# Kernel tuning notes

Hardware: AMD Instinct MI355X
Metric: run time of the kernel (lower is better)

Reference implementation:

```python
import jax, jax.numpy as jnp
import numpy as np

B, L, D, H = 4, 8192, 1024, 8
Dh = D // H
EPS = 1e-4
PAD = 1  # circular padding on each side, kernel_size=3, stride=1


def setup_inputs() -> dict:
    key = jax.random.key(0)
    k1, k2, k3, k4, k5 = jax.random.split(key, 5)
    return {
        "x": jax.random.normal(k1, (B, L, D), dtype=jnp.float32),
        "hash_w": jax.random.normal(k2, (H, Dh, 2), dtype=jnp.float32) * 0.05,
        "hash_b": jax.random.normal(k3, (H, 2), dtype=jnp.float32) * 0.05,
        "conv_w": jax.random.normal(k4, (D, D // H, 3), dtype=jnp.float32) * 0.05,
        "conv_b": jax.random.normal(k5, (D,), dtype=jnp.float32) * 0.05,
    }


def reference(x, hash_w, hash_b, conv_w, conv_b):
    # x: [B, L, D]
    xh = x.reshape(B, L, H, Dh)
    # per-head 2-dim hash projection, concatenated as [x0,y0,x1,y1,...] on last dim
    proj = jnp.einsum('blhd,hdk->blhk', xh, hash_w) + hash_b  # [B,L,H,2]
    proj = proj.reshape(B, L, 2 * H)
    # faithful to torch.split(projected, n_heads, dim=2): first H vs last H channels
    h_x, h_y = proj[..., :H], proj[..., H:]
    angles = jnp.arctan(h_x / (h_y + EPS))  # [B,L,H]
    idx = jnp.argsort(angles, axis=1)       # [B,L,H] permutation along L per (b,h)
    # gather: reorder tokens per head
    xs = jnp.take_along_axis(xh, idx[..., None], axis=1)  # [B,L,H,Dh]
    # grouped circular Conv1d over the sorted sequence
    xc = xs.reshape(B, L, D).swapaxes(1, 2)               # [B,D,L]
    xc = jnp.pad(xc, ((0, 0), (0, 0), (PAD, PAD)), mode='wrap')
    y = jax.lax.conv_general_dilated(
        xc, conv_w, window_strides=(1,), padding='VALID',
        dimension_numbers=('NCH', 'OIH', 'NCH'), feature_group_count=H)
    y = y + conv_b[None, :, None]                          # [B,D,L]
    y = y.swapaxes(1, 2).reshape(B, L, H, Dh)
    # scatter back to original token order == gather with inverse permutation
    inv = jnp.argsort(idx, axis=1)
    out = jnp.take_along_axis(y, inv[..., None], axis=1)
    return out.reshape(B, L, D)
```

## Files before the change

### kernel.cpp

```cpp
#include <hip/hip_runtime.h>
#include <math.h>

#define LL 8192
#define DD 1024
#define DH 128

typedef unsigned long long u64;
typedef __attribute__((ext_vector_type(8))) short bf16x8;
typedef __attribute__((ext_vector_type(4))) float f32x4;

__device__ __forceinline__ unsigned short f2bf(float f) {
  unsigned u = __float_as_uint(f);
  u = (u + 0x7fffu + ((u >> 16) & 1u)) >> 16;
  return (unsigned short)u;
}

__device__ __forceinline__ float fdlibm_atanf(float x) {
#pragma clang fp contract(off)
  const float atanhi0 = __uint_as_float(0x3eed6338u);
  const float atanhi1 = __uint_as_float(0x3f490fdau);
  const float atanhi2 = __uint_as_float(0x3f7b985eu);
  const float atanhi3 = __uint_as_float(0x3fc90fdau);
  const float atanlo0 = __uint_as_float(0x31ac3769u);
  const float atanlo1 = __uint_as_float(0x33222168u);
  const float atanlo2 = __uint_as_float(0x33140fb4u);
  const float atanlo3 = __uint_as_float(0x33a22168u);
  const float aT0 = __uint_as_float(0x3eaaaaa9u);
  const float aT1 = __uint_as_float(0xbe4cca98u);
  const float aT2 = __uint_as_float(0x3e11f50du);
  const float aT3 = __uint_as_float(0xbdda1247u);
  const float aT4 = __uint_as_float(0x3d7cac25u);
  unsigned hx = __float_as_uint(x);
  unsigned ix = hx & 0x7fffffffu;
  int id;
  if (ix >= 0x4c800000u) {
    if (ix > 0x7f800000u) return x + x;
    float z = atanhi3 + atanlo3;
    return (hx >> 31) ? -z : z;
  }
  if (ix < 0x3ee00000u) {
    if (ix < 0x39800000u) return x;
    id = -1;
  } else {
    x = fabsf(x);
    if (ix < 0x3f980000u) {
      if (ix < 0x3f300000u) { id = 0; x = (2.0f * x - 1.0f) / (2.0f + x); }
      else                  { id = 1; x = (x - 1.0f) / (x + 1.0f); }
    } else {
      if (ix < 0x401c0000u) { id = 2; x = (x - 1.5f) / (1.0f + 1.5f * x); }
      else                  { id = 3; x = -1.0f / x; }
    }
  }
  float z = x * x;
  float w = z * z;
  float s1 = z * (aT0 + w * (aT2 + w * aT4));
  float s2 = w * (aT1 + w * aT3);
  if (id < 0) return x - x * (s1 + s2);
  float r;
  if (id == 0)      r = atanhi0 - ((x * (s1 + s2) - atanlo0) - x);
  else if (id == 1) r = atanhi1 - ((x * (s1 + s2) - atanlo1) - x);
  else if (id == 2) r = atanhi2 - ((x * (s1 + s2) - atanlo2) - x);
  else              r = atanhi3 - ((x * (s1 + s2) - atanlo3) - x);
  return (hx >> 31) ? -r : r;
}

__global__ __launch_bounds__(256) void k_keys(const float* __restrict__ x,
                                              const float* __restrict__ hw,
                                              const float* __restrict__ hb,
                                              u64* __restrict__ ks,
                                              const float* __restrict__ cw,
                                              unsigned short* __restrict__ wb) {
  __shared__ float2 wL[128][8];
  __shared__ float projL[32][16];
  const int tid = threadIdx.x;
  const float2* hw2 = (const float2*)hw;
  for (int i = tid; i < 1024; i += 256) {
    int hh = i >> 7, dd = i & 127;
    wL[dd][hh] = hw2[i];
  }
  __syncthreads();
  const int r = tid >> 3;
  const int h = tid & 7;
  const int m = blockIdx.x * 32 + r;
  const float4* xp = (const float4*)(x + (size_t)m * DD + h * DH);
  float a0 = 0.f, a1 = 0.f;
#pragma unroll
  for (int q = 0; q < 32; ++q) {
    float4 v = xp[q];
    float2 w0 = wL[q * 4 + 0][h];
    float2 w1 = wL[q * 4 + 1][h];
    float2 w2 = wL[q * 4 + 2][h];
    float2 w3 = wL[q * 4 + 3][h];
    a0 = fmaf(v.x, w0.x, a0); a1 = fmaf(v.x, w0.y, a1);
    a0 = fmaf(v.y, w1.x, a0); a1 = fmaf(v.y, w1.y, a1);
    a0 = fmaf(v.z, w2.x, a0); a1 = fmaf(v.z, w2.y, a1);
    a0 = fmaf(v.w, w3.x, a0); a1 = fmaf(v.w, w3.y, a1);
  }
  projL[r][h * 2 + 0] = a0;
  projL[r][h * 2 + 1] = a1;
  __syncthreads();
  const int j = h;
  float px = projL[r][j] + hb[j];
  float py = projL[r][8 + j] + hb[8 + j];
  float den = py + 1e-4f;
  float ratio = px / den;
  float angle = fdlibm_atanf(ratio);
  unsigned am = __float_as_uint(angle);
  am = (am & 0x80000000u) ? ~am : (am | 0x80000000u);
  const int b = m >> 13, l = m & (LL - 1);
  ks[((size_t)b * 8 + j) * LL + l] = ((u64)am << 13) | (u64)l;
  {
    int base = blockIdx.x * 384;
    for (int g = base + tid; g < base + 384; g += 256) {
      int hh = g / 49152;
      int rem = g % 49152;
      int kk = rem >> 12;
      int rem2 = rem & 4095;
      int n = rem2 >> 9;
      int rem3 = rem2 & 511;
      int l2 = rem3 >> 3;
      int j2 = rem3 & 7;
      int k = kk * 32 + ((l2 >> 4) * 8) + j2;
      int o = n * 16 + (l2 & 15);
      int t = k >> 7, i2 = k & 127;
      wb[g] = f2bf(cw[((size_t)(hh * 128 + o)) * 384 + i2 * 3 + t]);
    }
  }
}

__global__ __launch_bounds__(256) void k_sort_loc512(u64* __restrict__ ks) {
  __shared__ u64 sk[512];
  const int blk = blockIdx.x;
  const int seg = blk >> 4, c = blk & 15;
  u64* base = ks + (size_t)seg * LL + c * 512;
  const int tid = threadIdx.x;
  sk[tid] = base[tid];
  sk[tid + 256] = base[tid + 256];
  __syncthreads();
  const int cb = c * 512;
  for (int size = 2; size <= 512; size <<= 1) {
    for (int stride = size >> 1; stride > 0; stride >>= 1) {
      int i = 2 * tid - (tid & (stride - 1));
      int j = i + stride;
      bool up = (((cb + i) & size) == 0);
      u64 a = sk[i], d = sk[j];
      if ((a > d) == up) { sk[i] = d; sk[j] = a; }
      __syncthreads();
    }
  }
  base[tid] = sk[tid];
  base[tid + 256] = sk[tid + 256];
}

__global__ __launch_bounds__(1024) void k_sort_loc2k(u64* __restrict__ ks) {
  __shared__ u64 sk[2048];
  const int blk = blockIdx.x;
  const int seg = blk >> 2, c = blk & 3;
  u64* base = ks + (size_t)seg * LL + c * 2048;
  const int tid = threadIdx.x;
  sk[tid] = base[tid];
  sk[tid + 1024] = base[tid + 1024];
  __syncthreads();
  const int cb = c * 2048;
  for (int size = 1024; size <= 2048; size <<= 1) {
    for (int stride = size >> 1; stride > 0; stride >>= 1) {
      int i = 2 * tid - (tid & (stride - 1));
      int j = i + stride;
      bool up = (((cb + i) & size) == 0);
      u64 a = sk[i], d = sk[j];
      if ((a > d) == up) { sk[i] = d; sk[j] = a; }
      __syncthreads();
    }
  }
  base[tid] = sk[tid];
  base[tid + 1024] = sk[tid + 1024];
}

__global__ __launch_bounds__(1024) void k_sort_t4k(u64* __restrict__ ks) {
  __shared__ u64 sk[4096];
  const int blk = blockIdx.x;
  const int seg = blk >> 1, c = blk & 1;
  u64* base = ks + (size_t)seg * LL + c * 4096;
  const int tid = threadIdx.x;
#pragma unroll
  for (int i = 0; i < 4; ++i) sk[tid + i * 1024] = base[tid + i * 1024];
  __syncthreads();
  const int cb = c * 4096;
  for (int stride = 2048; stride > 0; stride >>= 1) {
#pragma unroll
    for (int pp = 0; pp < 2; ++pp) {
      int p = tid + pp * 1024;
      int i = 2 * p - (p & (stride - 1));
      int j = i + stride;
      bool up = (((cb + i) & 4096) == 0);
      u64 a = sk[i], d = sk[j];
      if ((a > d) == up) { sk[i] = d; sk[j] = a; }
    }
    __syncthreads();
  }
#pragma unroll
  for (int i = 0; i < 4; ++i) base[tid + i * 1024] = sk[tid + i * 1024];
}

__global__ __launch_bounds__(256) void k_sort_g8(u64* __restrict__ ks) {
  int t = blockIdx.x * 256 + threadIdx.x;
  int seg = t >> 11, i = t & 2047;
  u64* base = ks + (size_t)seg * LL;
  u64 e0 = base[i], e1 = base[i + 2048], e2 = base[i + 4096], e3 = base[i + 6144];
  u64 tt;
  if (e0 > e2) { tt = e0; e0 = e2; e2 = tt; }
  if (e1 > e3) { tt = e1; e1 = e3; e3 = tt; }
  if (e0 > e1) { tt = e0; e0 = e1; e1 = tt; }
  if (e2 > e3) { tt = e2; e2 = e3; e3 = tt; }
  base[i] = e0; base[i + 2048] = e1; base[i + 4096] = e2; base[i + 6144] = e3;
}

__global__ __launch_bounds__(1024) void k_sort_tail(u64* __restrict__ ks,
                                                    int size,
                                                    int* __restrict__ perm) {
  __shared__ u64 sk[2048];
  const int blk = blockIdx.x;
  const int seg = blk >> 2, c = blk & 3;
  u64* base = ks + (size_t)seg * LL + c * 2048;
  const int tid = threadIdx.x;
  sk[tid] = base[tid];
  sk[tid + 1024] = base[tid + 1024];
  __syncthreads();
  const int cb = c * 2048;
  for (int stride = 1024; stride > 0; stride >>= 1) {
    int i = 2 * tid - (tid & (stride - 1));
    int j = i + stride;
    bool up = (((cb + i) & size) == 0);
    u64 a = sk[i], d = sk[j];
    if ((a > d) == up) { sk[i] = d; sk[j] = a; }
    __syncthreads();
  }
  if (perm) {
    int* dst = perm + (size_t)seg * LL + c * 2048;
    dst[tid] = (int)(sk[tid] & (u64)(LL - 1));
    dst[tid + 1024] = (int)(sk[tid + 1024] & (u64)(LL - 1));
  } else {
    base[tid] = sk[tid];
    base[tid + 1024] = sk[tid + 1024];
  }
}

__global__ __launch_bounds__(256) void k_conv(const float* __restrict__ x,
                                              const unsigned short* __restrict__ wb,
                                              const float* __restrict__ bias,
                                              const int* __restrict__ perm,
                                              float* __restrict__ out) {
  __shared__ short Xs[66 * 136];
  __shared__ short Ws[8 * 64 * 8];
  __shared__ int Ps[64];
  const int tid = threadIdx.x;
  const int bid = blockIdx.x;
  const int tile = bid & 127;
  const int h = (bid >> 7) & 7;
  const int b = bid >> 10;
  const int r0 = tile * 64;
  const int* pbh = perm + ((size_t)b * 8 + h) * LL;
  if (tid < 64) Ps[tid] = pbh[r0 + tid];
  {
    const int ln = tid & 31;
    for (int j = (tid >> 5); j < 66; j += 8) {
      int rank = (r0 + j - 1 + LL) & (LL - 1);
      int src = pbh[rank];
      float4 v = ((const float4*)(x + ((size_t)(b * LL + src)) * DD + h * DH))[ln];
      uint2 pk;
      pk.x = (unsigned)f2bf(v.x) | ((unsigned)f2bf(v.y) << 16);
      pk.y = (unsigned)f2bf(v.z) | ((unsigned)f2bf(v.w) << 16);
      *(uint2*)(Xs + j * 136 + ln * 4) = pk;
    }
  }
  const int w = tid >> 6;
  const int l = tid & 63;
  const int arow = w * 16 + (l & 15);
  const int acol = (l >> 4) * 8;
  f32x4 acc[8];
#pragma unroll
  for (int n = 0; n < 8; ++n) acc[n] = (f32x4){0.f, 0.f, 0.f, 0.f};
  const uint4* wsrc = (const uint4*)(wb + (size_t)h * 49152);
  uint4* Ws16 = (uint4*)Ws;
  for (int kk = 0; kk < 12; ++kk) {
    __syncthreads();
    Ws16[tid] = wsrc[kk * 512 + tid];
    Ws16[tid + 256] = wsrc[kk * 512 + tid + 256];
    __syncthreads();
    bf16x8 af = *(const bf16x8*)(Xs + (arow + (kk >> 2)) * 136 + (kk & 3) * 32 + acol);
#pragma unroll
    for (int n = 0; n < 8; ++n) {
      bf16x8 bf_ = *(const bf16x8*)(Ws + (n * 64 + l) * 8);
      acc[n] = __builtin_amdgcn_mfma_f32_16x16x32_bf16(af, bf_, acc[n], 0, 0, 0);
    }
  }
  int dsts[4];
#pragma unroll
  for (int reg = 0; reg < 4; ++reg) dsts[reg] = Ps[w * 16 + (l >> 4) * 4 + reg];
#pragma unroll
  for (int n = 0; n < 8; ++n) {
    int o = h * DH + n * 16 + (l & 15);
    float bv = bias[o];
#pragma unroll
    for (int reg = 0; reg < 4; ++reg) {
      out[((size_t)(b * LL + dsts[reg])) * DD + o] = acc[n][reg] + bv;
    }
  }
}

extern "C" void kernel_launch(void* const* d_in, const int* in_sizes, int n_in,
                              void* d_out, int out_size, void* d_ws, size_t ws_size,
                              hipStream_t stream) {
  const float* x  = (const float*)d_in[0];
  const float* hw = (const float*)d_in[1];
  const float* hb = (const float*)d_in[2];
  const float* cw = (const float*)d_in[3];
  const float* cb = (const float*)d_in[4];
  float* out = (float*)d_out;
  u64* ks   = (u64*)d_ws;
  int* perm = (int*)((char*)d_ws + (2u << 20));
  unsigned short* wbp = (unsigned short*)((char*)d_ws + (3u << 20));

  k_keys<<<1024, 256, 0, stream>>>(x, hw, hb, ks, cw, wbp);
  k_sort_loc512<<<512, 256, 0, stream>>>(ks);
  k_sort_loc2k<<<128, 1024, 0, stream>>>(ks);
  k_sort_t4k<<<64, 1024, 0, stream>>>(ks);
  k_sort_g8<<<256, 256, 0, stream>>>(ks);
  k_sort_tail<<<128, 1024, 0, stream>>>(ks, 8192, perm);
  k_conv<<<4096, 256, 0, stream>>>(x, wbp, cb, perm, out);
}
```

Baseline: 122.4 us.

## Cache bf16 head-major copy of x in keys kernel for conv gather

The keys kernel already streams all of x, so it now also writes a bf16 copy laid out by [batch, head, token, dim] into workspace. The conv kernel then gathers permuted rows from this half-size contiguous buffer instead of re-reading fp32 rows strided by DD and converting them. The permutation indices are also preloaded into shared memory once and reused for both the gather and the scatter. The cost is an extra 32 MB write in the keys kernel, and the fast path only runs if the workspace is large enough.

```diff
diff --git a/kernel.cpp b/kernel.cpp
--- a/kernel.cpp
+++ b/kernel.cpp
@@ -64,12 +64,14 @@
   return (hx >> 31) ? -r : r;
 }
 
+template <int XC>
 __global__ __launch_bounds__(256) void k_keys(const float* __restrict__ x,
                                               const float* __restrict__ hw,
                                               const float* __restrict__ hb,
                                               u64* __restrict__ ks,
                                               const float* __restrict__ cw,
-                                              unsigned short* __restrict__ wb) {
+                                              unsigned short* __restrict__ wb,
+                                              unsigned short* __restrict__ xc) {
   __shared__ float2 wL[128][8];
   __shared__ float projL[32][16];
   const int tid = threadIdx.x;
@@ -82,11 +84,19 @@
   const int r = tid >> 3;
   const int h = tid & 7;
   const int m = blockIdx.x * 32 + r;
+  const int b = m >> 13, l = m & (LL - 1);
   const float4* xp = (const float4*)(x + (size_t)m * DD + h * DH);
+  unsigned short* xcp = XC ? (xc + (((size_t)(b * 8 + h)) * LL + l) * DH) : nullptr;
   float a0 = 0.f, a1 = 0.f;
 #pragma unroll
   for (int q = 0; q < 32; ++q) {
     float4 v = xp[q];
+    if (XC) {
+      uint2 pk;
+      pk.x = (unsigned)f2bf(v.x) | ((unsigned)f2bf(v.y) << 16);
+      pk.y = (unsigned)f2bf(v.z) | ((unsigned)f2bf(v.w) << 16);
+      *(uint2*)(xcp + q * 4) = pk;
+    }
     float2 w0 = wL[q * 4 + 0][h];
     float2 w1 = wL[q * 4 + 1][h];
     float2 w2 = wL[q * 4 + 2][h];
@@ -107,7 +117,6 @@
   float angle = fdlibm_atanf(ratio);
   unsigned am = __float_as_uint(angle);
   am = (am & 0x80000000u) ? ~am : (am | 0x80000000u);
-  const int b = m >> 13, l = m & (LL - 1);
   ks[((size_t)b * 8 + j) * LL + l] = ((u64)am << 13) | (u64)l;
   {
     int base = blockIdx.x * 384;
@@ -245,14 +254,16 @@
   }
 }
 
+template <int XC>
 __global__ __launch_bounds__(256) void k_conv(const float* __restrict__ x,
+                                              const unsigned short* __restrict__ xc,
                                               const unsigned short* __restrict__ wb,
                                               const float* __restrict__ bias,
                                               const int* __restrict__ perm,
                                               float* __restrict__ out) {
   __shared__ short Xs[66 * 136];
   __shared__ short Ws[8 * 64 * 8];
-  __shared__ int Ps[64];
+  __shared__ int Ps2[66];
   const int tid = threadIdx.x;
   const int bid = blockIdx.x;
   const int tile = bid & 127;
@@ -260,17 +271,25 @@
   const int b = bid >> 10;
   const int r0 = tile * 64;
   const int* pbh = perm + ((size_t)b * 8 + h) * LL;
-  if (tid < 64) Ps[tid] = pbh[r0 + tid];
+  if (tid < 66) Ps2[tid] = pbh[(r0 + tid - 1 + LL) & (LL - 1)];
+  __syncthreads();
   {
     const int ln = tid & 31;
-    for (int j = (tid >> 5); j < 66; j += 8) {
-      int rank = (r0 + j - 1 + LL) & (LL - 1);
-      int src = pbh[rank];
-      float4 v = ((const float4*)(x + ((size_t)(b * LL + src)) * DD + h * DH))[ln];
-      uint2 pk;
-      pk.x = (unsigned)f2bf(v.x) | ((unsigned)f2bf(v.y) << 16);
-      pk.y = (unsigned)f2bf(v.z) | ((unsigned)f2bf(v.w) << 16);
-      *(uint2*)(Xs + j * 136 + ln * 4) = pk;
+    if (XC) {
+      const unsigned short* xcb = xc + ((size_t)(b * 8 + h)) * LL * DH;
+      for (int j = (tid >> 5); j < 66; j += 8) {
+        const uint2* sp = (const uint2*)(xcb + (size_t)Ps2[j] * DH);
+        *(uint2*)(Xs + j * 136 + ln * 4) = sp[ln];
+      }
+    } else {
+      for (int j = (tid >> 5); j < 66; j += 8) {
+        int src = Ps2[j];
+        float4 v = ((const float4*)(x + ((size_t)(b * LL + src)) * DD + h * DH))[ln];
+        uint2 pk;
+        pk.x = (unsigned)f2bf(v.x) | ((unsigned)f2bf(v.y) << 16);
+        pk.y = (unsigned)f2bf(v.z) | ((unsigned)f2bf(v.w) << 16);
+        *(uint2*)(Xs + j * 136 + ln * 4) = pk;
+      }
     }
   }
   const int w = tid >> 6;
@@ -296,7 +315,7 @@
   }
   int dsts[4];
 #pragma unroll
-  for (int reg = 0; reg < 4; ++reg) dsts[reg] = Ps[w * 16 + (l >> 4) * 4 + reg];
+  for (int reg = 0; reg < 4; ++reg) dsts[reg] = Ps2[1 + w * 16 + (l >> 4) * 4 + reg];
 #pragma unroll
   for (int n = 0; n < 8; ++n) {
     int o = h * DH + n * 16 + (l & 15);
@@ -320,12 +339,18 @@
   u64* ks   = (u64*)d_ws;
   int* perm = (int*)((char*)d_ws + (2u << 20));
   unsigned short* wbp = (unsigned short*)((char*)d_ws + (3u << 20));
-
-  k_keys<<<1024, 256, 0, stream>>>(x, hw, hb, ks, cw, wbp);
+  const size_t XC_OFF = (size_t)4 << 20;
+  const size_t XC_BYTES = (size_t)4 * 8 * LL * DH * 2;
+  bool use_xc = ws_size >= XC_OFF + XC_BYTES;
+  unsigned short* xcp = (unsigned short*)((char*)d_ws + XC_OFF);
+
+  if (use_xc) k_keys<1><<<1024, 256, 0, stream>>>(x, hw, hb, ks, cw, wbp, xcp);
+  else        k_keys<0><<<1024, 256, 0, stream>>>(x, hw, hb, ks, cw, wbp, nullptr);
   k_sort_loc512<<<512, 256, 0, stream>>>(ks);
   k_sort_loc2k<<<128, 1024, 0, stream>>>(ks);
   k_sort_t4k<<<64, 1024, 0, stream>>>(ks);
   k_sort_g8<<<256, 256, 0, stream>>>(ks);
   k_sort_tail<<<128, 1024, 0, stream>>>(ks, 8192, perm);
-  k_conv<<<4096, 256, 0, stream>>>(x, wbp, cb, perm, out);
-}
+  if (use_xc) k_conv<1><<<4096, 256, 0, stream>>>(x, xcp, wbp, cb, perm, out);
+  else        k_conv<0><<<4096, 256, 0, stream>>>(x, nullptr, wbp, cb, perm, out);
+}
```

After: 158.7 us. 1.3x slower.

## Fuse final bitonic merge stage into tail sort and prefetch conv weights

Applied to the files above, without the earlier changes.

Merges the stride-2048/4096 global compare-exchange kernel into the tail sort kernel. Each block recomputes the 4-element network from global memory and keeps only its own quarter, which removes one launch and one round trip of the keys through global memory. In the conv kernel, the 66 permutation indices are staged once in shared memory and reused for the gather and the scatter. Weight tiles are register-prefetched one k-step ahead so global load latency overlaps the MFMA work. The cost is redundant global reads of keys across the four blocks per segment, and higher register pressure in the conv kernel.

```diff
diff --git a/kernel.cpp b/kernel.cpp
--- a/kernel.cpp
+++ b/kernel.cpp
@@ -9,10 +9,10 @@
 typedef __attribute__((ext_vector_type(8))) short bf16x8;
 typedef __attribute__((ext_vector_type(4))) float f32x4;
 
-__device__ __forceinline__ unsigned short f2bf(float f) {
+__device__ __forceinline__ unsigned f2bf(float f) {
   unsigned u = __float_as_uint(f);
   u = (u + 0x7fffu + ((u >> 16) & 1u)) >> 16;
-  return (unsigned short)u;
+  return u;
 }
 
 __device__ __forceinline__ float fdlibm_atanf(float x) {
@@ -82,6 +82,7 @@
   const int r = tid >> 3;
   const int h = tid & 7;
   const int m = blockIdx.x * 32 + r;
+  const int b = m >> 13, l = m & (LL - 1);
   const float4* xp = (const float4*)(x + (size_t)m * DD + h * DH);
   float a0 = 0.f, a1 = 0.f;
 #pragma unroll
@@ -107,7 +108,6 @@
   float angle = fdlibm_atanf(ratio);
   unsigned am = __float_as_uint(angle);
   am = (am & 0x80000000u) ? ~am : (am | 0x80000000u);
-  const int b = m >> 13, l = m & (LL - 1);
   ks[((size_t)b * 8 + j) * LL + l] = ((u64)am << 13) | (u64)l;
   {
     int base = blockIdx.x * 384;
@@ -123,7 +123,7 @@
       int k = kk * 32 + ((l2 >> 4) * 8) + j2;
       int o = n * 16 + (l2 & 15);
       int t = k >> 7, i2 = k & 127;
-      wb[g] = f2bf(cw[((size_t)(hh * 128 + o)) * 384 + i2 * 3 + t]);
+      wb[g] = (unsigned short)f2bf(cw[((size_t)(hh * 128 + o)) * 384 + i2 * 3 + t]);
     }
   }
 }
@@ -202,47 +202,35 @@
   for (int i = 0; i < 4; ++i) base[tid + i * 1024] = sk[tid + i * 1024];
 }
 
-__global__ __launch_bounds__(256) void k_sort_g8(u64* __restrict__ ks) {
-  int t = blockIdx.x * 256 + threadIdx.x;
-  int seg = t >> 11, i = t & 2047;
-  u64* base = ks + (size_t)seg * LL;
-  u64 e0 = base[i], e1 = base[i + 2048], e2 = base[i + 4096], e3 = base[i + 6144];
-  u64 tt;
-  if (e0 > e2) { tt = e0; e0 = e2; e2 = tt; }
-  if (e1 > e3) { tt = e1; e1 = e3; e3 = tt; }
-  if (e0 > e1) { tt = e0; e0 = e1; e1 = tt; }
-  if (e2 > e3) { tt = e2; e2 = e3; e3 = tt; }
-  base[i] = e0; base[i + 2048] = e1; base[i + 4096] = e2; base[i + 6144] = e3;
-}
-
-__global__ __launch_bounds__(1024) void k_sort_tail(u64* __restrict__ ks,
-                                                    int size,
-                                                    int* __restrict__ perm) {
+__global__ __launch_bounds__(1024) void k_sort_tailg8(const u64* __restrict__ ks,
+                                                      int* __restrict__ perm) {
   __shared__ u64 sk[2048];
   const int blk = blockIdx.x;
   const int seg = blk >> 2, c = blk & 3;
-  u64* base = ks + (size_t)seg * LL + c * 2048;
-  const int tid = threadIdx.x;
-  sk[tid] = base[tid];
-  sk[tid + 1024] = base[tid + 1024];
-  __syncthreads();
-  const int cb = c * 2048;
+  const u64* base = ks + (size_t)seg * LL;
+  const int tid = threadIdx.x;
+#pragma unroll
+  for (int s = 0; s < 2; ++s) {
+    int i = tid + s * 1024;
+    u64 e0 = base[i], e1 = base[i + 2048], e2 = base[i + 4096], e3 = base[i + 6144];
+    u64 tt;
+    if (e0 > e2) { tt = e0; e0 = e2; e2 = tt; }
+    if (e1 > e3) { tt = e1; e1 = e3; e3 = tt; }
+    if (e0 > e1) { tt = e0; e0 = e1; e1 = tt; }
+    if (e2 > e3) { tt = e2; e2 = e3; e3 = tt; }
+    sk[i] = (c == 0) ? e0 : (c == 1) ? e1 : (c == 2) ? e2 : e3;
+  }
+  __syncthreads();
   for (int stride = 1024; stride > 0; stride >>= 1) {
     int i = 2 * tid - (tid & (stride - 1));
     int j = i + stride;
-    bool up = (((cb + i) & size) == 0);
     u64 a = sk[i], d = sk[j];
-    if ((a > d) == up) { sk[i] = d; sk[j] = a; }
+    if (a > d) { sk[i] = d; sk[j] = a; }
     __syncthreads();
   }
-  if (perm) {
-    int* dst = perm + (size_t)seg * LL + c * 2048;
-    dst[tid] = (int)(sk[tid] & (u64)(LL - 1));
-    dst[tid + 1024] = (int)(sk[tid + 1024] & (u64)(LL - 1));
-  } else {
-    base[tid] = sk[tid];
-    base[tid + 1024] = sk[tid + 1024];
-  }
+  int* dst = perm + (size_t)seg * LL + c * 2048;
+  dst[tid] = (int)(sk[tid] & (u64)(LL - 1));
+  dst[tid + 1024] = (int)(sk[tid + 1024] & (u64)(LL - 1));
 }
 
 __global__ __launch_bounds__(256) void k_conv(const float* __restrict__ x,
@@ -252,7 +240,7 @@
                                               float* __restrict__ out) {
   __shared__ short Xs[66 * 136];
   __shared__ short Ws[8 * 64 * 8];
-  __shared__ int Ps[64];
+  __shared__ int Ps2[66];
   const int tid = threadIdx.x;
   const int bid = blockIdx.x;
   const int tile = bid & 127;
@@ -260,16 +248,19 @@
   const int b = bid >> 10;
   const int r0 = tile * 64;
   const int* pbh = perm + ((size_t)b * 8 + h) * LL;
-  if (tid < 64) Ps[tid] = pbh[r0 + tid];
+  if (tid < 66) Ps2[tid] = pbh[(r0 + tid - 1 + LL) & (LL - 1)];
+  const uint4* wsrc = (const uint4*)(wb + (size_t)h * 49152);
+  uint4 wr0 = wsrc[tid];
+  uint4 wr1 = wsrc[tid + 256];
+  __syncthreads();
   {
     const int ln = tid & 31;
     for (int j = (tid >> 5); j < 66; j += 8) {
-      int rank = (r0 + j - 1 + LL) & (LL - 1);
-      int src = pbh[rank];
+      int src = Ps2[j];
       float4 v = ((const float4*)(x + ((size_t)(b * LL + src)) * DD + h * DH))[ln];
       uint2 pk;
-      pk.x = (unsigned)f2bf(v.x) | ((unsigned)f2bf(v.y) << 16);
-      pk.y = (unsigned)f2bf(v.z) | ((unsigned)f2bf(v.w) << 16);
+      pk.x = f2bf(v.x) | (f2bf(v.y) << 16);
+      pk.y = f2bf(v.z) | (f2bf(v.w) << 16);
       *(uint2*)(Xs + j * 136 + ln * 4) = pk;
     }
   }
@@ -280,13 +271,16 @@
   f32x4 acc[8];
 #pragma unroll
   for (int n = 0; n < 8; ++n) acc[n] = (f32x4){0.f, 0.f, 0.f, 0.f};
-  const uint4* wsrc = (const uint4*)(wb + (size_t)h * 49152);
   uint4* Ws16 = (uint4*)Ws;
   for (int kk = 0; kk < 12; ++kk) {
     __syncthreads();
-    Ws16[tid] = wsrc[kk * 512 + tid];
-    Ws16[tid + 256] = wsrc[kk * 512 + tid + 256];
+    Ws16[tid] = wr0;
+    Ws16[tid + 256] = wr1;
     __syncthreads();
+    if (kk < 11) {
+      wr0 = wsrc[(kk + 1) * 512 + tid];
+      wr1 = wsrc[(kk + 1) * 512 + tid + 256];
+    }
     bf16x8 af = *(const bf16x8*)(Xs + (arow + (kk >> 2)) * 136 + (kk & 3) * 32 + acol);
 #pragma unroll
     for (int n = 0; n < 8; ++n) {
@@ -296,7 +290,7 @@
   }
   int dsts[4];
 #pragma unroll
-  for (int reg = 0; reg < 4; ++reg) dsts[reg] = Ps[w * 16 + (l >> 4) * 4 + reg];
+  for (int reg = 0; reg < 4; ++reg) dsts[reg] = Ps2[1 + w * 16 + (l >> 4) * 4 + reg];
 #pragma unroll
   for (int n = 0; n < 8; ++n) {
     int o = h * DH + n * 16 + (l & 15);
@@ -325,7 +319,6 @@
   k_sort_loc512<<<512, 256, 0, stream>>>(ks);
   k_sort_loc2k<<<128, 1024, 0, stream>>>(ks);
   k_sort_t4k<<<64, 1024, 0, stream>>>(ks);
-  k_sort_g8<<<256, 256, 0, stream>>>(ks);
-  k_sort_tail<<<128, 1024, 0, stream>>>(ks, 8192, perm);
+  k_sort_tailg8<<<128, 1024, 0, stream>>>(ks, perm);
   k_conv<<<4096, 256, 0, stream>>>(x, wbp, cb, perm, out);
 }
```

Result: faster. 118.3 us (-3.4%).
